# Kernel optimization log

Measured on AMD Instinct MI355X. Metric: run time of the kernel, lower is better.

The kernel has to match this reference:

```python
import jax, jax.numpy as jnp
import numpy as np

N = 50000          # num nodes
E = 800000         # num edges (before self-loops)
F_IN = 128
H = 4              # heads
C1 = 16            # hidden channels per head
C2 = 8             # out channels per head
NEG_SLOPE = 0.2
EPS = 1e-16


def setup_inputs() -> dict:
    key = jax.random.key(0)
    ks = jax.random.split(key, 10)
    x = jax.random.normal(ks[0], (N, F_IN), dtype=jnp.float32)
    edge_index = jax.random.randint(ks[1], (2, E), 0, N, dtype=jnp.int64)
    s1 = 1.0 / np.sqrt(F_IN)
    s2 = 1.0 / np.sqrt(H * C1)
    return {
        "x": x,
        "edge_index": edge_index,
        "W1": jax.random.normal(ks[2], (F_IN, H * C1), dtype=jnp.float32) * s1,
        "a_src1": jax.random.normal(ks[3], (H, C1), dtype=jnp.float32) * s2,
        "a_dst1": jax.random.normal(ks[4], (H, C1), dtype=jnp.float32) * s2,
        "b1": jnp.zeros((H * C1,), dtype=jnp.float32),
        "W2": jax.random.normal(ks[5], (H * C1, H * C2), dtype=jnp.float32) * s2,
        "a_src2": jax.random.normal(ks[6], (H, C2), dtype=jnp.float32) * 0.2,
        "a_dst2": jax.random.normal(ks[7], (H, C2), dtype=jnp.float32) * 0.2,
        "b2": jnp.zeros((H * C2,), dtype=jnp.float32),
    }


def _gat_conv(x, src, dst, W, a_src, a_dst, b, heads, ch):
    # linear transform -> per-head features [N, H, C]
    h = (x @ W).reshape(-1, heads, ch)
    # per-node attention logits [N, H]
    al_src = jnp.sum(h * a_src[None], axis=-1)
    al_dst = jnp.sum(h * a_dst[None], axis=-1)
    # edge-wise logits + leaky relu [E, H]
    e = al_src[src] + al_dst[dst]
    e = jnp.where(e >= 0, e, NEG_SLOPE * e)
    # segment softmax over destination neighborhoods
    m = jax.ops.segment_max(e, dst, num_segments=N)
    e = jnp.exp(e - m[dst])
    s = jax.ops.segment_sum(e, dst, num_segments=N)
    alpha = e / (s[dst] + EPS)                      # [E, H]
    # weighted gather-scatter aggregate [N, H, C]
    msg = h[src] * alpha[..., None]
    out = jax.ops.segment_sum(msg, dst, num_segments=N)
    # concat heads + bias
    return out.reshape(-1, heads * ch) + b


def reference(x, edge_index, W1, a_src1, a_dst1, b1, W2, a_src2, a_dst2, b2):
    # PyG GATConv adds self-loops by default
    loop = jnp.arange(N, dtype=edge_index.dtype)
    src = jnp.concatenate([edge_index[0], loop])
    dst = jnp.concatenate([edge_index[1], loop])
    h = _gat_conv(x, src, dst, W1, a_src1, a_dst1, b1, H, C1)
    h = jax.nn.relu(h)
    h = _gat_conv(h, src, dst, W2, a_src2, a_dst2, b2, H, C2)
    return jax.nn.log_softmax(h, axis=1)
```

## Files before the change

### kernel.cpp

```cpp
#include <hip/hip_runtime.h>
#include <hip/hip_bf16.h>
#include <math.h>

#define NN 50000
#define NE 800000
#define ET (NE + NN)
#define DCAP 48
#define MAXOVF 8192
#define NG1 1563

__device__ __forceinline__ float bf2f(unsigned short u) {
    return __uint_as_float(((unsigned)u) << 16);
}
__device__ __forceinline__ unsigned short f2bf(float f) {
    unsigned u = __float_as_uint(f);
    return (unsigned short)((u + 0x7fff + ((u >> 16) & 1)) >> 16);
}
__device__ __forceinline__ float lrelu(float e) {
    return e >= 0.f ? e : 0.2f * e;
}

__global__ __launch_bounds__(256) void k_gemm1cv(const void* __restrict__ xraw,
                                                 const void* __restrict__ ei,
                                                 const void* p2, const void* p3, const void* p4, const void* p5,
                                                 const void* p6, const void* p7, const void* p8, const void* p9,
                                                 unsigned short* __restrict__ h1b,
                                                 float* __restrict__ als, float* __restrict__ ald,
                                                 int* __restrict__ csrF, int* __restrict__ deg,
                                                 int2* __restrict__ ovf, int* __restrict__ ovfcnt,
                                                 float* __restrict__ wsm) {
    __shared__ unsigned int Wp[64 * 65];
    __shared__ float xt[32 * 132];
    __shared__ int wred[8];
    int tid = threadIdx.x;
    int rb = blockIdx.x * 32;

    const unsigned long long* e64u = (const unsigned long long*)ei;
    const unsigned int* x32 = (const unsigned int*)xraw;
    int ci = 0, cf = 0;
    #pragma unroll
    for (int q = 0; q < 4; q++) {
        if (e64u[4 * tid + q] >= (unsigned long long)NN) ci = 1;
        unsigned ex = (x32[4 * tid + q] >> 7) & 0xFFu;
        cf += (ex >= 96 && ex <= 140) ? 1 : 0;
    }
    #pragma unroll
    for (int off = 32; off; off >>= 1) { ci |= __shfl_xor(ci, off); cf += __shfl_xor(cf, off); }
    if ((tid & 63) == 0) { wred[tid >> 6] = ci; wred[4 + (tid >> 6)] = cf; }
    __syncthreads();
    int iflag = (wred[0] | wred[1] | wred[2] | wred[3]) ? 0 : 1;
    int fl = ((wred[4] + wred[5] + wred[6] + wred[7]) > 700) ? 1 : 0;

    const void* w1raw = p2; const void* as1raw = p3; const void* ad1raw = p4;
    for (int i = tid; i < 64 * 64; i += 256) {
        int k2 = i >> 6, c = i & 63;
        unsigned lo, hi;
        if (fl) {
            lo = ((const unsigned short*)w1raw)[(2 * k2) * 64 + c];
            hi = ((const unsigned short*)w1raw)[(2 * k2 + 1) * 64 + c];
        } else {
            lo = f2bf(((const float*)w1raw)[(2 * k2) * 64 + c]);
            hi = f2bf(((const float*)w1raw)[(2 * k2 + 1) * 64 + c]);
        }
        Wp[c * 65 + k2] = lo | (hi << 16);
    }
    if (fl) {
        const unsigned short* xb = (const unsigned short*)xraw;
        for (int i = tid; i < 32 * 16; i += 256) {
            int r = i >> 4, k8 = i & 15;
            float f[8];
            if (rb + r < NN) {
                uint4 v = ((const uint4*)xb)[(size_t)(rb + r) * 16 + k8];
                f[0] = bf2f((unsigned short)(v.x & 0xffff)); f[1] = bf2f((unsigned short)(v.x >> 16));
                f[2] = bf2f((unsigned short)(v.y & 0xffff)); f[3] = bf2f((unsigned short)(v.y >> 16));
                f[4] = bf2f((unsigned short)(v.z & 0xffff)); f[5] = bf2f((unsigned short)(v.z >> 16));
                f[6] = bf2f((unsigned short)(v.w & 0xffff)); f[7] = bf2f((unsigned short)(v.w >> 16));
            } else {
                #pragma unroll
                for (int q = 0; q < 8; q++) f[q] = 0.f;
            }
            int o = r * 132 + k8 * 8;
            *(float4*)&xt[o]     = make_float4(f[0], f[1], f[2], f[3]);
            *(float4*)&xt[o + 4] = make_float4(f[4], f[5], f[6], f[7]);
        }
    } else {
        const float* xf = (const float*)xraw;
        for (int i = tid; i < 32 * 32; i += 256) {
            int r = i >> 5, kq = i & 31;
            float4 v = make_float4(0.f, 0.f, 0.f, 0.f);
            if (rb + r < NN) v = ((const float4*)xf)[(size_t)(rb + r) * 32 + kq];
            *(float4*)&xt[r * 132 + kq * 4] = v;
        }
    }
    __syncthreads();
    int c = tid & 63;
    int rg = tid >> 6;
    float acc[8];
    #pragma unroll
    for (int j = 0; j < 8; j++) acc[j] = 0.f;
    for (int k2 = 0; k2 < 64; k2 += 2) {
        unsigned q0 = Wp[c * 65 + k2];
        unsigned q1 = Wp[c * 65 + k2 + 1];
        float w0 = __uint_as_float(q0 << 16);
        float w1 = __uint_as_float(q0 & 0xffff0000u);
        float w2 = __uint_as_float(q1 << 16);
        float w3 = __uint_as_float(q1 & 0xffff0000u);
        int kk = k2 * 2;
        #pragma unroll
        for (int j = 0; j < 8; j++) {
            float4 xv = *(const float4*)&xt[(rg * 8 + j) * 132 + kk];
            acc[j] = fmaf(xv.x, w0, fmaf(xv.y, w1, fmaf(xv.z, w2, fmaf(xv.w, w3, acc[j]))));
        }
    }
    float asf = fl ? bf2f(((const unsigned short*)as1raw)[c]) : ((const float*)as1raw)[c];
    float adf = fl ? bf2f(((const unsigned short*)ad1raw)[c]) : ((const float*)ad1raw)[c];
    #pragma unroll
    for (int j = 0; j < 8; j++) {
        int r = rb + rg * 8 + j;
        bool ok = r < NN;
        if (ok) h1b[(size_t)r * 64 + c] = f2bf(acc[j]);
        float v = acc[j] * asf, w = acc[j] * adf;
        #pragma unroll
        for (int off = 1; off < 16; off <<= 1) {
            v += __shfl_xor(v, off);
            w += __shfl_xor(w, off);
        }
        if (ok && (c & 15) == 0) {
            als[r * 4 + (c >> 4)] = v;
            ald[r * 4 + (c >> 4)] = w;
        }
    }

    const long long* e64s = (const long long*)ei;
    for (int e = blockIdx.x * 256 + tid; e < ET; e += NG1 * 256) {
        if (e < 10528) {
            const void* p; int off;
            if (e < 8192)       { p = p2; off = e; }
            else if (e < 8256)  { p = p3; off = e - 8192; }
            else if (e < 8320)  { p = p4; off = e - 8256; }
            else if (e < 8384)  { p = p5; off = e - 8320; }
            else if (e < 10432) { p = p6; off = e - 8384; }
            else if (e < 10464) { p = p7; off = e - 10432; }
            else if (e < 10496) { p = p8; off = e - 10464; }
            else                { p = p9; off = e - 10496; }
            wsm[e] = fl ? bf2f(((const unsigned short*)p)[off]) : ((const float*)p)[off];
        }
        int s, d;
        if (e >= NE) { s = d = e - NE; }
        else if (iflag) {
            s = (int)e64s[e];
            d = (int)e64s[NE + e];
        } else {
            s = ((const int*)ei)[e];
            d = ((const int*)ei)[NE + e];
        }
        int slot = atomicAdd(&deg[d], 1);
        if (slot < DCAP) csrF[(size_t)d * DCAP + slot] = s;
        else {
            int o = atomicAdd(ovfcnt, 1);
            if (o < MAXOVF) ovf[o] = make_int2(s, d);
        }
    }
}

__global__ __launch_bounds__(256) void k_agg1(const int* __restrict__ degv, const int* __restrict__ csrF,
                                              const int2* __restrict__ ovf, const int* __restrict__ ovfcnt,
                                              const float* __restrict__ als, const float* __restrict__ aldv,
                                              const unsigned short* __restrict__ h1b,
                                              const float* __restrict__ b1,
                                              float* __restrict__ out1) {
    __shared__ float pv[4][DCAP * 4];
    __shared__ int  sidx[4][DCAP];
    int w = threadIdx.x >> 6, lane = threadIdx.x & 63;
    int n = blockIdx.x * 4 + w;
    if (n >= NN) return;
    int dg = degv[n];
    const int* cf = csrF + (size_t)n * DCAP;
    float4 ald = *(const float4*)(aldv + 4 * n);

    if (dg <= DCAP) {
        int sA = 0;
        bool v0 = lane < dg;
        if (v0) {
            sA = cf[lane];
            sidx[w][lane] = sA;
            float4 a = *(const float4*)(als + 4 * sA);
            float4 p;
            p.x = __expf(lrelu(a.x + ald.x)); p.y = __expf(lrelu(a.y + ald.y));
            p.z = __expf(lrelu(a.z + ald.z)); p.w = __expf(lrelu(a.w + ald.w));
            *(float4*)&pv[w][lane * 4] = p;
        }
        int degp = (dg + 3) & ~3;
        int s0v = __shfl(sA, 0);
        if (lane >= dg && lane < degp) {
            sidx[w][lane] = s0v;
            *(float4*)&pv[w][lane * 4] = make_float4(0.f, 0.f, 0.f, 0.f);
        }
        int g = lane >> 4, j = lane & 15, hh = j >> 2;
        float4 a4 = make_float4(0.f, 0.f, 0.f, 0.f);
        float ps = 0.f;
        for (int e = 0; e < degp; e += 4) {
            int s = sidx[w][e + g];
            float ph = pv[w][(e + g) * 4 + hh];
            uint2 rv = *(const uint2*)&h1b[(size_t)s * 64 + j * 4];
            ps += ph;
            a4.x = fmaf(ph, bf2f((unsigned short)(rv.x & 0xffff)), a4.x);
            a4.y = fmaf(ph, bf2f((unsigned short)(rv.x >> 16)),    a4.y);
            a4.z = fmaf(ph, bf2f((unsigned short)(rv.y & 0xffff)), a4.z);
            a4.w = fmaf(ph, bf2f((unsigned short)(rv.y >> 16)),    a4.w);
        }
        #pragma unroll
        for (int off = 16; off <= 32; off <<= 1) {
            a4.x += __shfl_xor(a4.x, off);
            a4.y += __shfl_xor(a4.y, off);
            a4.z += __shfl_xor(a4.z, off);
            a4.w += __shfl_xor(a4.w, off);
            ps   += __shfl_xor(ps,   off);
        }
        if (g == 0) {
            float rh = 1.f / (ps + 1e-16f);
            float4 bb = *(const float4*)&b1[j * 4];
            float4 o;
            o.x = fmaxf(a4.x * rh + bb.x, 0.f);
            o.y = fmaxf(a4.y * rh + bb.y, 0.f);
            o.z = fmaxf(a4.z * rh + bb.z, 0.f);
            o.w = fmaxf(a4.w * rh + bb.w, 0.f);
            *(float4*)&out1[(size_t)n * 64 + j * 4] = o;
        }
    } else {
        int h = lane >> 4;
        int oN = min(*ovfcnt, MAXOVF);
        float s0 = 0.f, s1 = 0.f, s2 = 0.f, s3 = 0.f;
        for (int i = lane; i < DCAP; i += 64) {
            int s = cf[i];
            float4 a = *(const float4*)(als + 4 * s);
            s0 += __expf(lrelu(a.x + ald.x));
            s1 += __expf(lrelu(a.y + ald.y));
            s2 += __expf(lrelu(a.z + ald.z));
            s3 += __expf(lrelu(a.w + ald.w));
        }
        for (int i = lane; i < oN; i += 64) {
            int2 pr = ovf[i];
            if (pr.y == n) {
                float4 a = *(const float4*)(als + 4 * pr.x);
                s0 += __expf(lrelu(a.x + ald.x));
                s1 += __expf(lrelu(a.y + ald.y));
                s2 += __expf(lrelu(a.z + ald.z));
                s3 += __expf(lrelu(a.w + ald.w));
            }
        }
        #pragma unroll
        for (int off = 32; off; off >>= 1) {
            s0 += __shfl_xor(s0, off);
            s1 += __shfl_xor(s1, off);
            s2 += __shfl_xor(s2, off);
            s3 += __shfl_xor(s3, off);
        }
        float sh = (h == 0) ? s0 : (h == 1) ? s1 : (h == 2) ? s2 : s3;
        float ah = (h == 0) ? ald.x : (h == 1) ? ald.y : (h == 2) ? ald.z : ald.w;
        float rh = 1.f / (sh + 1e-16f);
        float acc = 0.f;
        for (int e = 0; e < DCAP; ++e) {
            int s = cf[e];
            float av = als[4 * s + h];
            float ph = __expf(lrelu(av + ah));
            acc = fmaf(ph, bf2f(h1b[(size_t)s * 64 + lane]), acc);
        }
        for (int o = 0; o < oN; ++o) {
            int2 pr = ovf[o];
            if (pr.y == n) {
                float av = als[4 * pr.x + h];
                float ph = __expf(lrelu(av + ah));
                acc = fmaf(ph, bf2f(h1b[(size_t)pr.x * 64 + lane]), acc);
            }
        }
        out1[(size_t)n * 64 + lane] = fmaxf(acc * rh + b1[lane], 0.f);
    }
}

__global__ __launch_bounds__(256) void k_gemm2(const float* __restrict__ in,
                                               const float* __restrict__ Wf,
                                               const float* __restrict__ asf_p,
                                               const float* __restrict__ adf_p,
                                               unsigned short* __restrict__ h2b,
                                               float* __restrict__ als, float* __restrict__ ald) {
    __shared__ float Wt[32 * 65];
    __shared__ float xt[64 * 68];
    int tid = threadIdx.x;
    int rb = blockIdx.x * 64;
    for (int i = tid; i < 64 * 32; i += 256) {
        int k = i >> 5, c = i & 31;
        Wt[c * 65 + k] = Wf[i];
    }
    for (int i = tid; i < 64 * 16; i += 256) {
        int r = i >> 4, kq = i & 15;
        float4 v = make_float4(0.f, 0.f, 0.f, 0.f);
        if (rb + r < NN) v = ((const float4*)in)[(size_t)(rb + r) * 16 + kq];
        *(float4*)&xt[r * 68 + kq * 4] = v;
    }
    __syncthreads();
    int c = tid & 31, rg = tid >> 5;
    float acc[8];
    #pragma unroll
    for (int j = 0; j < 8; j++) acc[j] = 0.f;
    #pragma unroll 2
    for (int k = 0; k < 64; k += 4) {
        float4 w;
        w.x = Wt[c * 65 + k];     w.y = Wt[c * 65 + k + 1];
        w.z = Wt[c * 65 + k + 2]; w.w = Wt[c * 65 + k + 3];
        #pragma unroll
        for (int j = 0; j < 8; j++) {
            float4 xv = *(const float4*)&xt[(rg * 8 + j) * 68 + k];
            acc[j] = fmaf(xv.x, w.x, fmaf(xv.y, w.y, fmaf(xv.z, w.z, fmaf(xv.w, w.w, acc[j]))));
        }
    }
    float asf = asf_p[c], adf = adf_p[c];
    #pragma unroll
    for (int j = 0; j < 8; j++) {
        int r = rb + rg * 8 + j;
        bool ok = r < NN;
        if (ok) h2b[(size_t)r * 32 + c] = f2bf(acc[j]);
        float v = acc[j] * asf, w = acc[j] * adf;
        #pragma unroll
        for (int off = 1; off < 8; off <<= 1) {
            v += __shfl_xor(v, off);
            w += __shfl_xor(w, off);
        }
        if (ok && (c & 7) == 0) {
            als[r * 4 + (c >> 3)] = v;
            ald[r * 4 + (c >> 3)] = w;
        }
    }
}

__global__ __launch_bounds__(256) void k_agg2(const int* __restrict__ degv, const int* __restrict__ csrF,
                                              const int2* __restrict__ ovf, const int* __restrict__ ovfcnt,
                                              const float* __restrict__ als, const float* __restrict__ aldv,
                                              const unsigned short* __restrict__ h2b,
                                              const float* __restrict__ b2,
                                              float* __restrict__ out) {
    __shared__ float pv[4][DCAP * 4];
    __shared__ int  sidx[4][DCAP];
    int w = threadIdx.x >> 6, lane = threadIdx.x & 63;
    int n = blockIdx.x * 4 + w;
    if (n >= NN) return;
    int dg = degv[n];
    const int* cf = csrF + (size_t)n * DCAP;
    float4 ald = *(const float4*)(aldv + 4 * n);

    if (dg <= DCAP) {
        int sA = 0;
        bool v0 = lane < dg;
        if (v0) {
            sA = cf[lane];
            sidx[w][lane] = sA;
            float4 a = *(const float4*)(als + 4 * sA);
            float4 p;
            p.x = __expf(lrelu(a.x + ald.x)); p.y = __expf(lrelu(a.y + ald.y));
            p.z = __expf(lrelu(a.z + ald.z)); p.w = __expf(lrelu(a.w + ald.w));
            *(float4*)&pv[w][lane * 4] = p;
        }
        int degp = (dg + 7) & ~7;
        int s0v = __shfl(sA, 0);
        if (lane >= dg && lane < degp) {
            sidx[w][lane] = s0v;
            *(float4*)&pv[w][lane * 4] = make_float4(0.f, 0.f, 0.f, 0.f);
        }
        int g = lane >> 3, j = lane & 7, hh = j >> 1;
        float4 a4 = make_float4(0.f, 0.f, 0.f, 0.f);
        float ps = 0.f;
        for (int e = 0; e < degp; e += 8) {
            int s = sidx[w][e + g];
            float ph = pv[w][(e + g) * 4 + hh];
            uint2 rv = *(const uint2*)&h2b[(size_t)s * 32 + j * 4];
            ps += ph;
            a4.x = fmaf(ph, bf2f((unsigned short)(rv.x & 0xffff)), a4.x);
            a4.y = fmaf(ph, bf2f((unsigned short)(rv.x >> 16)),    a4.y);
            a4.z = fmaf(ph, bf2f((unsigned short)(rv.y & 0xffff)), a4.z);
            a4.w = fmaf(ph, bf2f((unsigned short)(rv.y >> 16)),    a4.w);
        }
        #pragma unroll
        for (int off = 8; off <= 32; off <<= 1) {
            a4.x += __shfl_xor(a4.x, off);
            a4.y += __shfl_xor(a4.y, off);
            a4.z += __shfl_xor(a4.z, off);
            a4.w += __shfl_xor(a4.w, off);
            ps   += __shfl_xor(ps,   off);
        }
        float rh = 1.f / (ps + 1e-16f);
        float4 bb = *(const float4*)&b2[j * 4];
        float4 row;
        row.x = a4.x * rh + bb.x; row.y = a4.y * rh + bb.y;
        row.z = a4.z * rh + bb.z; row.w = a4.w * rh + bb.w;
        float mx = fmaxf(fmaxf(row.x, row.y), fmaxf(row.z, row.w));
        #pragma unroll
        for (int off = 1; off < 8; off <<= 1) mx = fmaxf(mx, __shfl_xor(mx, off));
        float sm = __expf(row.x - mx) + __expf(row.y - mx)
                 + __expf(row.z - mx) + __expf(row.w - mx);
        #pragma unroll
        for (int off = 1; off < 8; off <<= 1) sm += __shfl_xor(sm, off);
        float lse = mx + logf(sm);
        if (g == 0) {
            float4 o;
            o.x = row.x - lse; o.y = row.y - lse;
            o.z = row.z - lse; o.w = row.w - lse;
            *(float4*)&out[(size_t)n * 32 + j * 4] = o;
        }
    } else {
        int oN = min(*ovfcnt, MAXOVF);
        float s0 = 0.f, s1 = 0.f, s2 = 0.f, s3 = 0.f;
        for (int i = lane; i < DCAP; i += 64) {
            int s = cf[i];
            float4 a = *(const float4*)(als + 4 * s);
            s0 += __expf(lrelu(a.x + ald.x));
            s1 += __expf(lrelu(a.y + ald.y));
            s2 += __expf(lrelu(a.z + ald.z));
            s3 += __expf(lrelu(a.w + ald.w));
        }
        for (int i = lane; i < oN; i += 64) {
            int2 pr = ovf[i];
            if (pr.y == n) {
                float4 a = *(const float4*)(als + 4 * pr.x);
                s0 += __expf(lrelu(a.x + ald.x));
                s1 += __expf(lrelu(a.y + ald.y));
                s2 += __expf(lrelu(a.z + ald.z));
                s3 += __expf(lrelu(a.w + ald.w));
            }
        }
        #pragma unroll
        for (int off = 32; off; off >>= 1) {
            s0 += __shfl_xor(s0, off);
            s1 += __shfl_xor(s1, off);
            s2 += __shfl_xor(s2, off);
            s3 += __shfl_xor(s3, off);
        }
        int L = lane & 31;
        int h2i = L >> 3;
        float sh2 = (h2i == 0) ? s0 : (h2i == 1) ? s1 : (h2i == 2) ? s2 : s3;
        float ah2 = (h2i == 0) ? ald.x : (h2i == 1) ? ald.y : (h2i == 2) ? ald.z : ald.w;
        float rh2 = 1.f / (sh2 + 1e-16f);
        if (lane < 32) {
            float acc = 0.f;
            for (int e = 0; e < DCAP; ++e) {
                int s = cf[e];
                float av = als[4 * s + h2i];
                float ph = __expf(lrelu(av + ah2));
                acc = fmaf(ph, bf2f(h2b[(size_t)s * 32 + L]), acc);
            }
            for (int o = 0; o < oN; ++o) {
                int2 pr = ovf[o];
                if (pr.y == n) {
                    float av = als[4 * pr.x + h2i];
                    float ph = __expf(lrelu(av + ah2));
                    acc = fmaf(ph, bf2f(h2b[(size_t)pr.x * 32 + L]), acc);
                }
            }
            float row = acc * rh2 + b2[L];
            float mx = row;
            #pragma unroll
            for (int off = 16; off; off >>= 1) mx = fmaxf(mx, __shfl_xor(mx, off, 32));
            float pe = __expf(row - mx);
            float sm = pe;
            #pragma unroll
            for (int off = 16; off; off >>= 1) sm += __shfl_xor(sm, off, 32);
            out[(size_t)n * 32 + L] = row - mx - logf(sm);
        }
    }
}

extern "C" void kernel_launch(void* const* d_in, const int* in_sizes, int n_in,
                              void* d_out, int out_size, void* d_ws, size_t ws_size,
                              hipStream_t stream) {
    const void* x  = d_in[0];
    const void* ei = d_in[1];
    float* out = (float*)d_out;

    char* p = (char*)d_ws;
    auto take = [&](size_t b) -> char* {
        char* r = p; p += (b + 255) & ~(size_t)255; return r;
    };
    int*   degc  = (int*)take(sizeof(int) * (NN + 8));
    int*   deg   = degc;
    int*   ovfcnt = degc + NN;
    int*   csrF  = (int*)take(sizeof(int) * (size_t)NN * DCAP);
    int2*  ovf   = (int2*)take(sizeof(int2) * MAXOVF);
    float* wsm   = (float*)take(sizeof(float) * 10528);
    unsigned short* h1b = (unsigned short*)take(sizeof(unsigned short) * (size_t)NN * 64);
    float* als1  = (float*)take(sizeof(float) * NN * 4);
    float* ald1  = (float*)take(sizeof(float) * NN * 4);
    float* out1  = (float*)take(sizeof(float) * (size_t)NN * 64);
    unsigned short* h2b = (unsigned short*)take(sizeof(unsigned short) * (size_t)NN * 32);
    float* als2  = (float*)take(sizeof(float) * NN * 4);
    float* ald2  = (float*)take(sizeof(float) * NN * 4);

    float* Wf2  = wsm + 8384;
    float* as2f = wsm + 10432;
    float* ad2f = wsm + 10464;
    float* b1f  = wsm + 8320;
    float* b2f  = wsm + 10496;

    hipMemsetAsync(degc, 0, sizeof(int) * (NN + 8), stream);
    k_gemm1cv<<<NG1, 256, 0, stream>>>(x, ei, d_in[2], d_in[3], d_in[4], d_in[5],
                                       d_in[6], d_in[7], d_in[8], d_in[9],
                                       h1b, als1, ald1, csrF, deg, ovf, ovfcnt, wsm);
    k_agg1<<<(NN + 3) / 4, 256, 0, stream>>>(deg, csrF, ovf, ovfcnt, als1, ald1, h1b, b1f, out1);
    k_gemm2<<<(NN + 63) / 64, 256, 0, stream>>>(out1, Wf2, as2f, ad2f, h2b, als2, ald2);
    k_agg2<<<(NN + 3) / 4, 256, 0, stream>>>(deg, csrF, ovf, ovfcnt, als2, ald2, h2b, b2f, out);
}
```

Baseline: 225.0 us.

## Split fused GEMM/CSR-build kernel and store CSR neighbor indices as 16-bit

The fused kernel that did the layer-1 GEMM and also built the bucketed CSR through atomics becomes two kernels. A standalone convert kernel with one thread per edge (3321 blocks) handles the CSR build and weight conversion, and a separate GEMM kernel computes h1 and the attention logits. CSR source indices are now stored as unsigned short, which halves the CSR footprint and the index traffic in both aggregation kernels. N=50000 fits in 16 bits, but this caps the node count, and the split adds one kernel launch and runs each kernel's input-format detection separately.

```diff
diff --git a/kernel.cpp b/kernel.cpp
--- a/kernel.cpp
+++ b/kernel.cpp
@@ -8,6 +8,7 @@
 #define DCAP 48
 #define MAXOVF 8192
 #define NG1 1563
+#define NCV 3321
 
 __device__ __forceinline__ float bf2f(unsigned short u) {
     return __uint_as_float(((unsigned)u) << 16);
@@ -20,47 +21,97 @@
     return e >= 0.f ? e : 0.2f * e;
 }
 
-__global__ __launch_bounds__(256) void k_gemm1cv(const void* __restrict__ xraw,
+__global__ __launch_bounds__(256) void k_convert(const void* __restrict__ xraw,
                                                  const void* __restrict__ ei,
                                                  const void* p2, const void* p3, const void* p4, const void* p5,
                                                  const void* p6, const void* p7, const void* p8, const void* p9,
-                                                 unsigned short* __restrict__ h1b,
-                                                 float* __restrict__ als, float* __restrict__ ald,
-                                                 int* __restrict__ csrF, int* __restrict__ deg,
+                                                 unsigned short* __restrict__ csrF, int* __restrict__ deg,
                                                  int2* __restrict__ ovf, int* __restrict__ ovfcnt,
                                                  float* __restrict__ wsm) {
-    __shared__ unsigned int Wp[64 * 65];
-    __shared__ float xt[32 * 132];
     __shared__ int wred[8];
-    int tid = threadIdx.x;
-    int rb = blockIdx.x * 32;
-
+    int t = threadIdx.x;
     const unsigned long long* e64u = (const unsigned long long*)ei;
     const unsigned int* x32 = (const unsigned int*)xraw;
     int ci = 0, cf = 0;
     #pragma unroll
     for (int q = 0; q < 4; q++) {
-        if (e64u[4 * tid + q] >= (unsigned long long)NN) ci = 1;
-        unsigned ex = (x32[4 * tid + q] >> 7) & 0xFFu;
+        if (e64u[4 * t + q] >= (unsigned long long)NN) ci = 1;
+        unsigned ex = (x32[4 * t + q] >> 7) & 0xFFu;
         cf += (ex >= 96 && ex <= 140) ? 1 : 0;
     }
     #pragma unroll
     for (int off = 32; off; off >>= 1) { ci |= __shfl_xor(ci, off); cf += __shfl_xor(cf, off); }
-    if ((tid & 63) == 0) { wred[tid >> 6] = ci; wred[4 + (tid >> 6)] = cf; }
+    if ((t & 63) == 0) { wred[t >> 6] = ci; wred[4 + (t >> 6)] = cf; }
     __syncthreads();
     int iflag = (wred[0] | wred[1] | wred[2] | wred[3]) ? 0 : 1;
     int fl = ((wred[4] + wred[5] + wred[6] + wred[7]) > 700) ? 1 : 0;
 
-    const void* w1raw = p2; const void* as1raw = p3; const void* ad1raw = p4;
+    int e = blockIdx.x * 256 + t;
+    if (e < 10528) {
+        const void* p; int off;
+        if (e < 8192)       { p = p2; off = e; }
+        else if (e < 8256)  { p = p3; off = e - 8192; }
+        else if (e < 8320)  { p = p4; off = e - 8256; }
+        else if (e < 8384)  { p = p5; off = e - 8320; }
+        else if (e < 10432) { p = p6; off = e - 8384; }
+        else if (e < 10464) { p = p7; off = e - 10432; }
+        else if (e < 10496) { p = p8; off = e - 10464; }
+        else                { p = p9; off = e - 10496; }
+        wsm[e] = fl ? bf2f(((const unsigned short*)p)[off]) : ((const float*)p)[off];
+    }
+    if (e >= ET) return;
+    int s, d;
+    if (e >= NE) { s = d = e - NE; }
+    else if (iflag) {
+        s = (int)((const long long*)ei)[e];
+        d = (int)((const long long*)ei)[NE + e];
+    } else {
+        s = ((const int*)ei)[e];
+        d = ((const int*)ei)[NE + e];
+    }
+    int slot = atomicAdd(&deg[d], 1);
+    if (slot < DCAP) csrF[(size_t)d * DCAP + slot] = (unsigned short)s;
+    else {
+        int o = atomicAdd(ovfcnt, 1);
+        if (o < MAXOVF) ovf[o] = make_int2(s, d);
+    }
+}
+
+__global__ __launch_bounds__(256) void k_gemm1(const void* __restrict__ xraw,
+                                               const void* __restrict__ w1raw,
+                                               const void* __restrict__ as1raw,
+                                               const void* __restrict__ ad1raw,
+                                               unsigned short* __restrict__ h1b,
+                                               float* __restrict__ als, float* __restrict__ ald) {
+    __shared__ unsigned int Wp[64 * 65];
+    __shared__ float xt[32 * 132];
+    __shared__ int wred[4];
+    int tid = threadIdx.x;
+    int rb = blockIdx.x * 32;
+
+    const unsigned int* x32 = (const unsigned int*)xraw;
+    int cf = 0;
+    #pragma unroll
+    for (int q = 0; q < 4; q++) {
+        unsigned ex = (x32[4 * tid + q] >> 7) & 0xFFu;
+        cf += (ex >= 96 && ex <= 140) ? 1 : 0;
+    }
+    #pragma unroll
+    for (int off = 32; off; off >>= 1) cf += __shfl_xor(cf, off);
+    if ((tid & 63) == 0) wred[tid >> 6] = cf;
+    __syncthreads();
+    int fl = ((wred[0] + wred[1] + wred[2] + wred[3]) > 700) ? 1 : 0;
+
+    const void* w1raw_ = w1raw; const void* as1raw_ = as1raw; const void* ad1raw_ = ad1raw;
     for (int i = tid; i < 64 * 64; i += 256) {
         int k2 = i >> 6, c = i & 63;
         unsigned lo, hi;
         if (fl) {
-            lo = ((const unsigned short*)w1raw)[(2 * k2) * 64 + c];
-            hi = ((const unsigned short*)w1raw)[(2 * k2 + 1) * 64 + c];
+            lo = ((const unsigned short*)w1raw_)[(2 * k2) * 64 + c];
+            hi = ((const unsigned short*)w1raw_)[(2 * k2 + 1) * 64 + c];
         } else {
-            lo = f2bf(((const float*)w1raw)[(2 * k2) * 64 + c]);
-            hi = f2bf(((const float*)w1raw)[(2 * k2 + 1) * 64 + c]);
+            lo = f2bf(((const float*)w1raw_)[(2 * k2) * 64 + c]);
+            hi = f2bf(((const float*)w1raw_)[(2 * k2 + 1) * 64 + c]);
         }
         Wp[c * 65 + k2] = lo | (hi << 16);
     }
@@ -112,8 +163,8 @@
             acc[j] = fmaf(xv.x, w0, fmaf(xv.y, w1, fmaf(xv.z, w2, fmaf(xv.w, w3, acc[j]))));
         }
     }
-    float asf = fl ? bf2f(((const unsigned short*)as1raw)[c]) : ((const float*)as1raw)[c];
-    float adf = fl ? bf2f(((const unsigned short*)ad1raw)[c]) : ((const float*)ad1raw)[c];
+    float asf = fl ? bf2f(((const unsigned short*)as1raw_)[c]) : ((const float*)as1raw_)[c];
+    float adf = fl ? bf2f(((const unsigned short*)ad1raw_)[c]) : ((const float*)ad1raw_)[c];
     #pragma unroll
     for (int j = 0; j < 8; j++) {
         int r = rb + rg * 8 + j;
@@ -130,40 +181,9 @@
             ald[r * 4 + (c >> 4)] = w;
         }
     }
-
-    const long long* e64s = (const long long*)ei;
-    for (int e = blockIdx.x * 256 + tid; e < ET; e += NG1 * 256) {
-        if (e < 10528) {
-            const void* p; int off;
-            if (e < 8192)       { p = p2; off = e; }
-            else if (e < 8256)  { p = p3; off = e - 8192; }
-            else if (e < 8320)  { p = p4; off = e - 8256; }
-            else if (e < 8384)  { p = p5; off = e - 8320; }
-            else if (e < 10432) { p = p6; off = e - 8384; }
-            else if (e < 10464) { p = p7; off = e - 10432; }
-            else if (e < 10496) { p = p8; off = e - 10464; }
-            else                { p = p9; off = e - 10496; }
-            wsm[e] = fl ? bf2f(((const unsigned short*)p)[off]) : ((const float*)p)[off];
-        }
-        int s, d;
-        if (e >= NE) { s = d = e - NE; }
-        else if (iflag) {
-            s = (int)e64s[e];
-            d = (int)e64s[NE + e];
-        } else {
-            s = ((const int*)ei)[e];
-            d = ((const int*)ei)[NE + e];
-        }
-        int slot = atomicAdd(&deg[d], 1);
-        if (slot < DCAP) csrF[(size_t)d * DCAP + slot] = s;
-        else {
-            int o = atomicAdd(ovfcnt, 1);
-            if (o < MAXOVF) ovf[o] = make_int2(s, d);
-        }
-    }
-}
-
-__global__ __launch_bounds__(256) void k_agg1(const int* __restrict__ degv, const int* __restrict__ csrF,
+}
+
+__global__ __launch_bounds__(256) void k_agg1(const int* __restrict__ degv, const unsigned short* __restrict__ csrF,
                                               const int2* __restrict__ ovf, const int* __restrict__ ovfcnt,
                                               const float* __restrict__ als, const float* __restrict__ aldv,
                                               const unsigned short* __restrict__ h1b,
@@ -175,7 +195,7 @@
     int n = blockIdx.x * 4 + w;
     if (n >= NN) return;
     int dg = degv[n];
-    const int* cf = csrF + (size_t)n * DCAP;
+    const unsigned short* cf = csrF + (size_t)n * DCAP;
     float4 ald = *(const float4*)(aldv + 4 * n);
 
     if (dg <= DCAP) {
@@ -333,7 +353,7 @@
     }
 }
 
-__global__ __launch_bounds__(256) void k_agg2(const int* __restrict__ degv, const int* __restrict__ csrF,
+__global__ __launch_bounds__(256) void k_agg2(const int* __restrict__ degv, const unsigned short* __restrict__ csrF,
                                               const int2* __restrict__ ovf, const int* __restrict__ ovfcnt,
                                               const float* __restrict__ als, const float* __restrict__ aldv,
                                               const unsigned short* __restrict__ h2b,
@@ -345,7 +365,7 @@
     int n = blockIdx.x * 4 + w;
     if (n >= NN) return;
     int dg = degv[n];
-    const int* cf = csrF + (size_t)n * DCAP;
+    const unsigned short* cf = csrF + (size_t)n * DCAP;
     float4 ald = *(const float4*)(aldv + 4 * n);
 
     if (dg <= DCAP) {
@@ -482,7 +502,7 @@
     int*   degc  = (int*)take(sizeof(int) * (NN + 8));
     int*   deg   = degc;
     int*   ovfcnt = degc + NN;
-    int*   csrF  = (int*)take(sizeof(int) * (size_t)NN * DCAP);
+    unsigned short* csrF = (unsigned short*)take(sizeof(unsigned short) * (size_t)NN * DCAP);
     int2*  ovf   = (int2*)take(sizeof(int2) * MAXOVF);
     float* wsm   = (float*)take(sizeof(float) * 10528);
     unsigned short* h1b = (unsigned short*)take(sizeof(unsigned short) * (size_t)NN * 64);
@@ -500,9 +520,10 @@
     float* b2f  = wsm + 10496;
 
     hipMemsetAsync(degc, 0, sizeof(int) * (NN + 8), stream);
-    k_gemm1cv<<<NG1, 256, 0, stream>>>(x, ei, d_in[2], d_in[3], d_in[4], d_in[5],
+    k_convert<<<NCV, 256, 0, stream>>>(x, ei, d_in[2], d_in[3], d_in[4], d_in[5],
                                        d_in[6], d_in[7], d_in[8], d_in[9],
-                                       h1b, als1, ald1, csrF, deg, ovf, ovfcnt, wsm);
+                                       csrF, deg, ovf, ovfcnt, wsm);
+    k_gemm1<<<NG1, 256, 0, stream>>>(x, d_in[2], d_in[3], d_in[4], h1b, als1, ald1);
     k_agg1<<<(NN + 3) / 4, 256, 0, stream>>>(deg, csrF, ovf, ovfcnt, als1, ald1, h1b, b1f, out1);
     k_gemm2<<<(NN + 63) / 64, 256, 0, stream>>>(out1, Wf2, as2f, ad2f, h2b, als2, ald2);
     k_agg2<<<(NN + 3) / 4, 256, 0, stream>>>(deg, csrF, ovf, ovfcnt, als2, ald2, h2b, b2f, out);
```

Measured after the change: 236.9 us. +5.3%, slower.

## Partition CSR build by destination range per XCD and store 16-bit neighbor ids

Applied to the files above, without the earlier changes.

The edge-scatter phase now splits destination nodes into 8 ranges keyed by blockIdx&7. Each group of 196 blocks scans all edges but only inserts those whose destination falls in its range. On MI355X consecutive block ids are typically spread across the XCDs, so the intent is to keep the degree atomics and CSR writes for a node range inside one XCD's L2. The CSR neighbor array also shrinks from int to unsigned short, which holds because node ids are below 65536, halving its write and read traffic in both aggregation kernels. The cost is that every partition re-reads the destination index array, giving 8x redundant index loads, and the weight-copy work is moved out of the edge loop.

```diff
diff --git a/kernel.cpp b/kernel.cpp
--- a/kernel.cpp
+++ b/kernel.cpp
@@ -7,7 +7,9 @@
 #define ET (NE + NN)
 #define DCAP 48
 #define MAXOVF 8192
-#define NG1 1563
+#define NG1R 1568
+#define NBP 196
+#define NRANGE 6250
 
 __device__ __forceinline__ float bf2f(unsigned short u) {
     return __uint_as_float(((unsigned)u) << 16);
@@ -26,7 +28,7 @@
                                                  const void* p6, const void* p7, const void* p8, const void* p9,
                                                  unsigned short* __restrict__ h1b,
                                                  float* __restrict__ als, float* __restrict__ ald,
-                                                 int* __restrict__ csrF, int* __restrict__ deg,
+                                                 unsigned short* __restrict__ csrF, int* __restrict__ deg,
                                                  int2* __restrict__ ovf, int* __restrict__ ovfcnt,
                                                  float* __restrict__ wsm) {
     __shared__ unsigned int Wp[64 * 65];
@@ -51,119 +53,128 @@
     int iflag = (wred[0] | wred[1] | wred[2] | wred[3]) ? 0 : 1;
     int fl = ((wred[4] + wred[5] + wred[6] + wred[7]) > 700) ? 1 : 0;
 
-    const void* w1raw = p2; const void* as1raw = p3; const void* ad1raw = p4;
-    for (int i = tid; i < 64 * 64; i += 256) {
-        int k2 = i >> 6, c = i & 63;
-        unsigned lo, hi;
+    if (rb < NN) {
+        const void* w1raw = p2; const void* as1raw = p3; const void* ad1raw = p4;
+        for (int i = tid; i < 64 * 64; i += 256) {
+            int k2 = i >> 6, c = i & 63;
+            unsigned lo, hi;
+            if (fl) {
+                lo = ((const unsigned short*)w1raw)[(2 * k2) * 64 + c];
+                hi = ((const unsigned short*)w1raw)[(2 * k2 + 1) * 64 + c];
+            } else {
+                lo = f2bf(((const float*)w1raw)[(2 * k2) * 64 + c]);
+                hi = f2bf(((const float*)w1raw)[(2 * k2 + 1) * 64 + c]);
+            }
+            Wp[c * 65 + k2] = lo | (hi << 16);
+        }
         if (fl) {
-            lo = ((const unsigned short*)w1raw)[(2 * k2) * 64 + c];
-            hi = ((const unsigned short*)w1raw)[(2 * k2 + 1) * 64 + c];
+            const unsigned short* xb = (const unsigned short*)xraw;
+            for (int i = tid; i < 32 * 16; i += 256) {
+                int r = i >> 4, k8 = i & 15;
+                float f[8];
+                if (rb + r < NN) {
+                    uint4 v = ((const uint4*)xb)[(size_t)(rb + r) * 16 + k8];
+                    f[0] = bf2f((unsigned short)(v.x & 0xffff)); f[1] = bf2f((unsigned short)(v.x >> 16));
+                    f[2] = bf2f((unsigned short)(v.y & 0xffff)); f[3] = bf2f((unsigned short)(v.y >> 16));
+                    f[4] = bf2f((unsigned short)(v.z & 0xffff)); f[5] = bf2f((unsigned short)(v.z >> 16));
+                    f[6] = bf2f((unsigned short)(v.w & 0xffff)); f[7] = bf2f((unsigned short)(v.w >> 16));
+                } else {
+                    #pragma unroll
+                    for (int q = 0; q < 8; q++) f[q] = 0.f;
+                }
+                int o = r * 132 + k8 * 8;
+                *(float4*)&xt[o]     = make_float4(f[0], f[1], f[2], f[3]);
+                *(float4*)&xt[o + 4] = make_float4(f[4], f[5], f[6], f[7]);
+            }
         } else {
-            lo = f2bf(((const float*)w1raw)[(2 * k2) * 64 + c]);
-            hi = f2bf(((const float*)w1raw)[(2 * k2 + 1) * 64 + c]);
-        }
-        Wp[c * 65 + k2] = lo | (hi << 16);
-    }
-    if (fl) {
-        const unsigned short* xb = (const unsigned short*)xraw;
-        for (int i = tid; i < 32 * 16; i += 256) {
-            int r = i >> 4, k8 = i & 15;
-            float f[8];
-            if (rb + r < NN) {
-                uint4 v = ((const uint4*)xb)[(size_t)(rb + r) * 16 + k8];
-                f[0] = bf2f((unsigned short)(v.x & 0xffff)); f[1] = bf2f((unsigned short)(v.x >> 16));
-                f[2] = bf2f((unsigned short)(v.y & 0xffff)); f[3] = bf2f((unsigned short)(v.y >> 16));
-                f[4] = bf2f((unsigned short)(v.z & 0xffff)); f[5] = bf2f((unsigned short)(v.z >> 16));
-                f[6] = bf2f((unsigned short)(v.w & 0xffff)); f[7] = bf2f((unsigned short)(v.w >> 16));
-            } else {
-                #pragma unroll
-                for (int q = 0; q < 8; q++) f[q] = 0.f;
-            }
-            int o = r * 132 + k8 * 8;
-            *(float4*)&xt[o]     = make_float4(f[0], f[1], f[2], f[3]);
-            *(float4*)&xt[o + 4] = make_float4(f[4], f[5], f[6], f[7]);
-        }
-    } else {
-        const float* xf = (const float*)xraw;
-        for (int i = tid; i < 32 * 32; i += 256) {
-            int r = i >> 5, kq = i & 31;
-            float4 v = make_float4(0.f, 0.f, 0.f, 0.f);
-            if (rb + r < NN) v = ((const float4*)xf)[(size_t)(rb + r) * 32 + kq];
-            *(float4*)&xt[r * 132 + kq * 4] = v;
-        }
-    }
-    __syncthreads();
-    int c = tid & 63;
-    int rg = tid >> 6;
-    float acc[8];
-    #pragma unroll
-    for (int j = 0; j < 8; j++) acc[j] = 0.f;
-    for (int k2 = 0; k2 < 64; k2 += 2) {
-        unsigned q0 = Wp[c * 65 + k2];
-        unsigned q1 = Wp[c * 65 + k2 + 1];
-        float w0 = __uint_as_float(q0 << 16);
-        float w1 = __uint_as_float(q0 & 0xffff0000u);
-        float w2 = __uint_as_float(q1 << 16);
-        float w3 = __uint_as_float(q1 & 0xffff0000u);
-        int kk = k2 * 2;
+            const float* xf = (const float*)xraw;
+            for (int i = tid; i < 32 * 32; i += 256) {
+                int r = i >> 5, kq = i & 31;
+                float4 v = make_float4(0.f, 0.f, 0.f, 0.f);
+                if (rb + r < NN) v = ((const float4*)xf)[(size_t)(rb + r) * 32 + kq];
+                *(float4*)&xt[r * 132 + kq * 4] = v;
+            }
+        }
+        __syncthreads();
+        int c = tid & 63;
+        int rg = tid >> 6;
+        float acc[8];
+        #pragma unroll
+        for (int j = 0; j < 8; j++) acc[j] = 0.f;
+        for (int k2 = 0; k2 < 64; k2 += 2) {
+            unsigned q0 = Wp[c * 65 + k2];
+            unsigned q1 = Wp[c * 65 + k2 + 1];
+            float w0 = __uint_as_float(q0 << 16);
+            float w1 = __uint_as_float(q0 & 0xffff0000u);
+            float w2 = __uint_as_float(q1 << 16);
+            float w3 = __uint_as_float(q1 & 0xffff0000u);
+            int kk = k2 * 2;
+            #pragma unroll
+            for (int j = 0; j < 8; j++) {
+                float4 xv = *(const float4*)&xt[(rg * 8 + j) * 132 + kk];
+                acc[j] = fmaf(xv.x, w0, fmaf(xv.y, w1, fmaf(xv.z, w2, fmaf(xv.w, w3, acc[j]))));
+            }
+        }
+        float asf = fl ? bf2f(((const unsigned short*)as1raw)[c]) : ((const float*)as1raw)[c];
+        float adf = fl ? bf2f(((const unsigned short*)ad1raw)[c]) : ((const float*)ad1raw)[c];
         #pragma unroll
         for (int j = 0; j < 8; j++) {
-            float4 xv = *(const float4*)&xt[(rg * 8 + j) * 132 + kk];
-            acc[j] = fmaf(xv.x, w0, fmaf(xv.y, w1, fmaf(xv.z, w2, fmaf(xv.w, w3, acc[j]))));
-        }
-    }
-    float asf = fl ? bf2f(((const unsigned short*)as1raw)[c]) : ((const float*)as1raw)[c];
-    float adf = fl ? bf2f(((const unsigned short*)ad1raw)[c]) : ((const float*)ad1raw)[c];
-    #pragma unroll
-    for (int j = 0; j < 8; j++) {
-        int r = rb + rg * 8 + j;
-        bool ok = r < NN;
-        if (ok) h1b[(size_t)r * 64 + c] = f2bf(acc[j]);
-        float v = acc[j] * asf, w = acc[j] * adf;
-        #pragma unroll
-        for (int off = 1; off < 16; off <<= 1) {
-            v += __shfl_xor(v, off);
-            w += __shfl_xor(w, off);
-        }
-        if (ok && (c & 15) == 0) {
-            als[r * 4 + (c >> 4)] = v;
-            ald[r * 4 + (c >> 4)] = w;
-        }
-    }
-
+            int r = rb + rg * 8 + j;
+            bool ok = r < NN;
+            if (ok) h1b[(size_t)r * 64 + c] = f2bf(acc[j]);
+            float v = acc[j] * asf, w = acc[j] * adf;
+            #pragma unroll
+            for (int off = 1; off < 16; off <<= 1) {
+                v += __shfl_xor(v, off);
+                w += __shfl_xor(w, off);
+            }
+            if (ok && (c & 15) == 0) {
+                als[r * 4 + (c >> 4)] = v;
+                ald[r * 4 + (c >> 4)] = w;
+            }
+        }
+    }
+
+    int ew = blockIdx.x * 256 + tid;
+    if (ew < 10528) {
+        const void* p; int off;
+        if (ew < 8192)       { p = p2; off = ew; }
+        else if (ew < 8256)  { p = p3; off = ew - 8192; }
+        else if (ew < 8320)  { p = p4; off = ew - 8256; }
+        else if (ew < 8384)  { p = p5; off = ew - 8320; }
+        else if (ew < 10432) { p = p6; off = ew - 8384; }
+        else if (ew < 10464) { p = p7; off = ew - 10432; }
+        else if (ew < 10496) { p = p8; off = ew - 10464; }
+        else                 { p = p9; off = ew - 10496; }
+        wsm[ew] = fl ? bf2f(((const unsigned short*)p)[off]) : ((const float*)p)[off];
+    }
+
+    int part = blockIdx.x & 7;
+    int bi = blockIdx.x >> 3;
+    int lo = part * NRANGE, hi = lo + NRANGE;
     const long long* e64s = (const long long*)ei;
-    for (int e = blockIdx.x * 256 + tid; e < ET; e += NG1 * 256) {
-        if (e < 10528) {
-            const void* p; int off;
-            if (e < 8192)       { p = p2; off = e; }
-            else if (e < 8256)  { p = p3; off = e - 8192; }
-            else if (e < 8320)  { p = p4; off = e - 8256; }
-            else if (e < 8384)  { p = p5; off = e - 8320; }
-            else if (e < 10432) { p = p6; off = e - 8384; }
-            else if (e < 10464) { p = p7; off = e - 10432; }
-            else if (e < 10496) { p = p8; off = e - 10464; }
-            else                { p = p9; off = e - 10496; }
-            wsm[e] = fl ? bf2f(((const unsigned short*)p)[off]) : ((const float*)p)[off];
-        }
-        int s, d;
-        if (e >= NE) { s = d = e - NE; }
-        else if (iflag) {
-            s = (int)e64s[e];
-            d = (int)e64s[NE + e];
-        } else {
-            s = ((const int*)ei)[e];
-            d = ((const int*)ei)[NE + e];
-        }
-        int slot = atomicAdd(&deg[d], 1);
-        if (slot < DCAP) csrF[(size_t)d * DCAP + slot] = s;
-        else {
-            int o = atomicAdd(ovfcnt, 1);
-            if (o < MAXOVF) ovf[o] = make_int2(s, d);
-        }
-    }
-}
-
-__global__ __launch_bounds__(256) void k_agg1(const int* __restrict__ degv, const int* __restrict__ csrF,
+    const int* e32s = (const int*)ei;
+    for (int e = bi * 256 + tid; e < ET; e += NBP * 256) {
+        int d;
+        if (e >= NE) d = e - NE;
+        else if (iflag) d = (int)e64s[NE + e];
+        else d = e32s[NE + e];
+        if (d >= lo && d < hi) {
+            int s;
+            if (e >= NE) s = d;
+            else if (iflag) s = (int)e64s[e];
+            else s = e32s[e];
+            int slot = atomicAdd(&deg[d], 1);
+            if (slot < DCAP) csrF[(size_t)d * DCAP + slot] = (unsigned short)s;
+            else {
+                int o = atomicAdd(ovfcnt, 1);
+                if (o < MAXOVF) ovf[o] = make_int2(s, d);
+            }
+        }
+    }
+}
+
+__global__ __launch_bounds__(256) void k_agg1(const int* __restrict__ degv, const unsigned short* __restrict__ csrF,
                                               const int2* __restrict__ ovf, const int* __restrict__ ovfcnt,
                                               const float* __restrict__ als, const float* __restrict__ aldv,
                                               const unsigned short* __restrict__ h1b,
@@ -175,7 +186,7 @@
     int n = blockIdx.x * 4 + w;
     if (n >= NN) return;
     int dg = degv[n];
-    const int* cf = csrF + (size_t)n * DCAP;
+    const unsigned short* cf = csrF + (size_t)n * DCAP;
     float4 ald = *(const float4*)(aldv + 4 * n);
 
     if (dg <= DCAP) {
@@ -333,7 +344,7 @@
     }
 }
 
-__global__ __launch_bounds__(256) void k_agg2(const int* __restrict__ degv, const int* __restrict__ csrF,
+__global__ __launch_bounds__(256) void k_agg2(const int* __restrict__ degv, const unsigned short* __restrict__ csrF,
                                               const int2* __restrict__ ovf, const int* __restrict__ ovfcnt,
                                               const float* __restrict__ als, const float* __restrict__ aldv,
                                               const unsigned short* __restrict__ h2b,
@@ -345,7 +356,7 @@
     int n = blockIdx.x * 4 + w;
     if (n >= NN) return;
     int dg = degv[n];
-    const int* cf = csrF + (size_t)n * DCAP;
+    const unsigned short* cf = csrF + (size_t)n * DCAP;
     float4 ald = *(const float4*)(aldv + 4 * n);
 
     if (dg <= DCAP) {
@@ -482,7 +493,7 @@
     int*   degc  = (int*)take(sizeof(int) * (NN + 8));
     int*   deg   = degc;
     int*   ovfcnt = degc + NN;
-    int*   csrF  = (int*)take(sizeof(int) * (size_t)NN * DCAP);
+    unsigned short* csrF = (unsigned short*)take(sizeof(unsigned short) * (size_t)NN * DCAP);
     int2*  ovf   = (int2*)take(sizeof(int2) * MAXOVF);
     float* wsm   = (float*)take(sizeof(float) * 10528);
     unsigned short* h1b = (unsigned short*)take(sizeof(unsigned short) * (size_t)NN * 64);
@@ -500,9 +511,9 @@
     float* b2f  = wsm + 10496;
 
     hipMemsetAsync(degc, 0, sizeof(int) * (NN + 8), stream);
-    k_gemm1cv<<<NG1, 256, 0, stream>>>(x, ei, d_in[2], d_in[3], d_in[4], d_in[5],
-                                       d_in[6], d_in[7], d_in[8], d_in[9],
-                                       h1b, als1, ald1, csrF, deg, ovf, ovfcnt, wsm);
+    k_gemm1cv<<<NG1R, 256, 0, stream>>>(x, ei, d_in[2], d_in[3], d_in[4], d_in[5],
+                                        d_in[6], d_in[7], d_in[8], d_in[9],
+                                        h1b, als1, ald1, csrF, deg, ovf, ovfcnt, wsm);
     k_agg1<<<(NN + 3) / 4, 256, 0, stream>>>(deg, csrF, ovf, ovfcnt, als1, ald1, h1b, b1f, out1);
     k_gemm2<<<(NN + 63) / 64, 256, 0, stream>>>(out1, Wf2, as2f, ad2f, h2b, als2, ald2);
     k_agg2<<<(NN + 3) / 4, 256, 0, stream>>>(deg, csrF, ovf, ovfcnt, als2, ald2, h2b, b2f, out);
```

New measurement: 221.3 us (median of 2 runs). Within noise of the previous version (-1.6%).
